# Kernel optimization log

Hardware: AMD Instinct MI355X
Metric: run time of the kernel (lower is better)

Reference implementation:

```python
import jax, jax.numpy as jnp
import numpy as np

IMG = 224
PATCH_SIZE = 2      # stride of the output patch grid (output_size = H // PATCH_SIZE)
PATCH_PIXEL = 4     # samples per patch side (deformable resampling resolution)
EMBED = 192
OFFSET_EMBED = 2    # (dx, dy) per patch
IN_CH = 3
BATCH = 32


def setup_inputs() -> dict:
    key = jax.random.key(0)
    k1, k2, k3 = jax.random.split(key, 3)
    x = jax.random.normal(k1, (BATCH, IN_CH, IMG, IMG), jnp.float32)
    conv_w = jax.random.normal(k2, (EMBED, IN_CH, 3, 3), jnp.float32) * 0.05
    conv_b = jnp.zeros((EMBED,), jnp.float32)
    off_w = jax.random.normal(k3, (OFFSET_EMBED, EMBED), jnp.float32) * 0.02
    return {"x": x, "conv_w": conv_w, "conv_b": conv_b, "off_w": off_w}


def _bilinear_gather(img, ys, xs):
    # img: [B, C, H, W]; ys, xs: [B, P] float pixel coords. Border-clamped bilinear.
    B, C, H, W = img.shape
    y0 = jnp.floor(ys)
    x0 = jnp.floor(xs)
    wy = (ys - y0)[:, None, :]
    wx = (xs - x0)[:, None, :]
    y0i = jnp.clip(y0.astype(jnp.int32), 0, H - 1)
    y1i = jnp.clip(y0i + 1, 0, H - 1)
    x0i = jnp.clip(x0.astype(jnp.int32), 0, W - 1)
    x1i = jnp.clip(x0i + 1, 0, W - 1)
    flat = img.reshape(B, C, H * W)
    P = ys.shape[1]

    def g(yi, xi):
        idx = (yi * W + xi)[:, None, :]  # [B,1,P]
        return jnp.take_along_axis(flat, jnp.broadcast_to(idx, (B, C, P)), axis=2)

    v00 = g(y0i, x0i)
    v01 = g(y0i, x1i)
    v10 = g(y1i, x0i)
    v11 = g(y1i, x1i)
    return (v00 * (1 - wy) * (1 - wx) + v01 * (1 - wy) * wx
            + v10 * wy * (1 - wx) + v11 * wy * wx)  # [B,C,P]


def reference(x, conv_w, conv_b, off_w):
    B, C, H, W = x.shape
    # PatchEmbed: conv k3 s2 p1 -> flatten -> tokens [B, N, E]
    feat = jax.lax.conv_general_dilated(
        x, conv_w, window_strides=(2, 2), padding=((1, 1), (1, 1)),
        dimension_numbers=('NCHW', 'OIHW', 'NCHW')) + conv_b[None, :, None, None]
    Hf, Wf = feat.shape[2], feat.shape[3]
    tokens = feat.reshape(B, EMBED, Hf * Wf).transpose(0, 2, 1)  # [B,N,E]
    # offset predictor: GELU (exact) then bias-free linear
    pred = jax.nn.gelu(tokens, approximate=False) @ off_w.T      # [B,N,2]

    Ho, Wo = H // PATCH_SIZE, W // PATCH_SIZE  # == (Hf, Wf) by construction
    off = pred.reshape(B, Ho, Wo, OFFSET_EMBED) * PATCH_SIZE     # pixel-space offsets

    # Deformable patch resampling: each output patch samples a PATCH_PIXEL^2 grid
    # centered at its shifted patch center.
    cy = (jnp.arange(Ho, dtype=jnp.float32) + 0.5) * PATCH_SIZE
    cx = (jnp.arange(Wo, dtype=jnp.float32) + 0.5) * PATCH_SIZE
    local = ((jnp.arange(PATCH_PIXEL, dtype=jnp.float32) + 0.5) / PATCH_PIXEL
             * PATCH_SIZE - PATCH_SIZE / 2)
    ys = (cy[None, :, None, None, None] + off[..., 1][:, :, :, None, None]
          + local[None, None, None, :, None])
    xs = (cx[None, None, :, None, None] + off[..., 0][:, :, :, None, None]
          + local[None, None, None, None, :])
    shape5 = (B, Ho, Wo, PATCH_PIXEL, PATCH_PIXEL)
    ys = jnp.broadcast_to(ys, shape5).reshape(B, -1)
    xs = jnp.broadcast_to(xs, shape5).reshape(B, -1)

    sampled = _bilinear_gather(x, ys, xs)  # [B,C,Ho*Wo*pp*pp]
    out = sampled.reshape(B, C, Ho, Wo, PATCH_PIXEL, PATCH_PIXEL)
    out = out.transpose(0, 1, 2, 4, 3, 5).reshape(
        B, C, Ho * PATCH_PIXEL, Wo * PATCH_PIXEL)
    return out
```

## Files before the change

### kernel.cpp

```cpp
#include <hip/hip_runtime.h>

#define IMG   224
#define IMG2  (IMG * IMG)
#define HO    112
#define WO_   112
#define EMBED 192
#define BATCH 32
#define PPB   (HO * WO_)
#define NPOS  (BATCH * PPB)

#define OFFS_BYTES ((size_t)NPOS * 8)
#define BT_DWORDS  (768 * 4)
#define PK_BYTES   (BT_DWORDS * 4 + 16 * 24 * 4)

typedef __attribute__((ext_vector_type(8))) short short8;
typedef __attribute__((ext_vector_type(4))) float float4v;
typedef __attribute__((ext_vector_type(2))) float float2v;
typedef __attribute__((ext_vector_type(4))) unsigned uint4v;

__device__ __forceinline__ short f2bf(float f) {
    unsigned u = __builtin_bit_cast(unsigned, f);
    u += 0x7FFFu + ((u >> 16) & 1u);
    return (short)(u >> 16);
}
__device__ __forceinline__ unsigned pack2bf(float lo, float hi) {
    return (unsigned)(unsigned short)f2bf(lo)
         | ((unsigned)(unsigned short)f2bf(hi) << 16);
}

__device__ __forceinline__ unsigned cvt_pk_bf16(float lo, float hi) {
    unsigned r;
    asm("v_cvt_pk_bf16_f32 %0, %1, %2" : "=v"(r) : "v"(lo), "v"(hi));
    return r;
}

__device__ __forceinline__ float fast_gelu(float a) {
    float e = __builtin_amdgcn_exp2f(a * -2.45546507f);
    return a * __builtin_amdgcn_rcpf(1.0f + e);
}

__device__ __forceinline__ void resample_patch(
    const float* __restrict__ xb, float* __restrict__ ob,
    int ho, int wo, int px, float ofx, float ofy)
{
    float xs  = 2.0f * wo + 0.25f + 0.5f * px + ofx;
    float x0f = floorf(xs);
    float wx  = xs - x0f;
    int x0 = (int)x0f; x0 = min(max(x0, 0), IMG - 1);
    int xq = min(x0, IMG - 2);
    bool selx = (x0 > xq);
    int ocol = wo * 4 + px;

#pragma unroll
    for (int py = 0; py < 4; ++py) {
        float ys  = 2.0f * ho + 0.25f + 0.5f * py + ofy;
        float y0f = floorf(ys);
        float wy  = ys - y0f;
        int y0 = (int)y0f; y0 = min(max(y0, 0), IMG - 1);
        int dyo = (y0 < IMG - 1) ? IMG : 0;
        int rb = y0 * IMG + xq;
        int orow = (ho * 4 + py) * 448 + ocol;

#pragma unroll
        for (int c = 0; c < 3; ++c) {
            int v0 = rb + c * IMG2;
            int v1 = v0 + dyo;
            float A0 = xb[v0], A1 = xb[v0 + 1];
            float B0 = xb[v1], B1 = xb[v1 + 1];
            float v00 = selx ? A1 : A0;
            float v10 = selx ? B1 : B0;
            float top = fmaf(wx, A1 - v00, v00);
            float bot = fmaf(wx, B1 - v10, v10);
            ob[c * 200704 + orow] = fmaf(wy, bot - top, top);
        }
    }
}

__global__ void pack_kernel(const float* __restrict__ conv_w,
                            const float* __restrict__ conv_b,
                            const float* __restrict__ off_w,
                            unsigned* __restrict__ pk) {
    int tid = threadIdx.x;
    for (int t = tid; t < 768; t += 256) {
        int nt = t >> 6, quad = (t >> 4) & 3, col = t & 15;
        int ch = nt * 16 + col;
        uint4v d;
#pragma unroll
        for (int jj = 0; jj < 4; ++jj) {
            int k0 = quad * 8 + 2 * jj, k1 = k0 + 1;
            float v0 = (k0 < 27) ? conv_w[ch * 27 + k0]
                                 : ((k0 == 27) ? conv_b[ch] : 0.0f);
            float v1 = (k1 < 27) ? conv_w[ch * 27 + k1]
                                 : ((k1 == 27) ? conv_b[ch] : 0.0f);
            d[jj] = pack2bf(v0, v1);
        }
        ((uint4v*)pk)[t] = d;
    }
    float* ow = (float*)(pk + BT_DWORDS);
    for (int t = tid; t < 384; t += 256) {
        int col = t / 24, e = t % 24;
        float v = (e < 12) ? off_w[e * 16 + col]
                           : off_w[EMBED + (e - 12) * 16 + col];
        ow[t] = v * 2.0f;
    }
}

__global__ __launch_bounds__(256)
void offsets_kernel(const float* __restrict__ x,
                    const unsigned* __restrict__ pk,
                    float2v* __restrict__ offs) {
    const int lane = threadIdx.x & 63;
    const int wv   = threadIdx.x >> 6;
    const int col  = lane & 15;
    const int quad = lane >> 4;

    const int b = blockIdx.x / (PPB / 64);
    const int p = (blockIdx.x % (PPB / 64)) * 64 + wv * 16;
    const float* __restrict__ xb = x + (size_t)b * 3 * IMG2;

    int  offj[8];
    bool isr[8], k27[8];
#pragma unroll
    for (int j = 0; j < 8; ++j) {
        int k = quad * 8 + j;
        int c = k / 9, r9 = k % 9;
        int dy = r9 / 3, dx = r9 % 3;
        isr[j] = (k < 27);
        k27[j] = (k == 27);
        offj[j] = isr[j] ? (c * IMG2 + dy * IMG + dx) : 0;
    }

    const uint4v* bT = (const uint4v*)pk;
    short8 bfrag[12];
#pragma unroll
    for (int nt = 0; nt < 12; ++nt)
        bfrag[nt] = __builtin_bit_cast(short8, bT[(nt * 4 + quad) * 16 + col]);
    const float4v* oT = (const float4v*)(pk + BT_DWORDS) + col * 6;
    float4v w0 = oT[0], w1 = oT[1], w2 = oT[2];
    float4v w3 = oT[3], w4 = oT[4], w5 = oT[5];
    float owx[12], owy[12];
#pragma unroll
    for (int i = 0; i < 4; ++i) {
        owx[i] = w0[i]; owx[4 + i] = w1[i]; owx[8 + i] = w2[i];
        owy[i] = w3[i]; owy[4 + i] = w4[i]; owy[8 + i] = w5[i];
    }

    const int ho  = p / WO_;
    const int wo0 = p % WO_;
    int iy0 = 2 * ho - 1;
    int ixl = 2 * (wo0 + col) - 1;
    int base = iy0 * IMG + ixl;

    float v[8];
    if (ho > 0 && wo0 > 0) {
#pragma unroll
        for (int j = 0; j < 8; ++j) {
            float t = isr[j] ? xb[base + offj[j]] : 0.0f;
            v[j] = k27[j] ? 1.0f : t;
        }
    } else {
#pragma unroll
        for (int j = 0; j < 8; ++j) {
            int k  = quad * 8 + j;
            int r9 = k % 9;
            int dy = r9 / 3, dx = r9 % 3;
            bool ok = isr[j] && (iy0 + dy >= 0) && (ixl + dx >= 0);
            int ad = ok ? (base + offj[j]) : 0;
            float t = ok ? xb[ad] : 0.0f;
            v[j] = k27[j] ? 1.0f : t;
        }
    }
    uint4v au = {cvt_pk_bf16(v[0], v[1]), cvt_pk_bf16(v[2], v[3]),
                 cvt_pk_bf16(v[4], v[5]), cvt_pk_bf16(v[6], v[7])};
    short8 a = __builtin_bit_cast(short8, au);

    float ox[4] = {0, 0, 0, 0}, oy[4] = {0, 0, 0, 0};
#pragma unroll
    for (int nt = 0; nt < 12; ++nt) {
        float4v c = {0.0f, 0.0f, 0.0f, 0.0f};
        c = __builtin_amdgcn_mfma_f32_16x16x32_bf16(a, bfrag[nt], c, 0, 0, 0);
#pragma unroll
        for (int r = 0; r < 4; ++r) {
            float g = fast_gelu(c[r]);
            ox[r] = fmaf(g, owx[nt], ox[r]);
            oy[r] = fmaf(g, owy[nt], oy[r]);
        }
    }
#pragma unroll
    for (int d = 1; d < 16; d <<= 1) {
#pragma unroll
        for (int r = 0; r < 4; ++r) {
            ox[r] += __shfl_xor(ox[r], d, 64);
            oy[r] += __shfl_xor(oy[r], d, 64);
        }
    }

    int rsel = col & 3;
    float sx01 = (rsel & 1) ? ox[1] : ox[0];
    float sx23 = (rsel & 1) ? ox[3] : ox[2];
    float vx   = (rsel & 2) ? sx23 : sx01;
    float sy01 = (rsel & 1) ? oy[1] : oy[0];
    float sy23 = (rsel & 1) ? oy[3] : oy[2];
    float vy   = (rsel & 2) ? sy23 : sy01;
    if (col < 4) {
        int gpos = blockIdx.x * 64 + wv * 16 + quad * 4 + rsel;
        float2v o; o[0] = vx; o[1] = vy;
        offs[gpos] = o;
    }
}

__global__ __launch_bounds__(256, 8)
void resample_kernel(const float* __restrict__ x,
                     const float2v* __restrict__ offs,
                     float* __restrict__ out) {
    const int lane  = threadIdx.x & 63;
    const int wv    = threadIdx.x >> 6;
    const int patch = lane >> 2;
    const int px    = lane & 3;

    const int b  = blockIdx.x / (PPB / 64);
    const int sb = (blockIdx.x % (PPB / 64)) * 64 + wv * 16;
    const int ho  = sb / WO_;
    const int wo0 = sb % WO_;

    const float* __restrict__ xb = x + (size_t)b * 3 * IMG2;
    float* __restrict__ ob = out + (size_t)b * 3 * (448 * 448);

    float2v o = offs[blockIdx.x * 64 + wv * 16 + patch];
    resample_patch(xb, ob, ho, wo0 + patch, px, o[0], o[1]);
}

__global__ __launch_bounds__(128)
void fused_kernel(const float* __restrict__ x,
                  const float* __restrict__ conv_w,
                  const float* __restrict__ conv_b,
                  const float* __restrict__ off_w,
                  float* __restrict__ out) {
    const int lane = threadIdx.x & 63;
    const int wv   = threadIdx.x >> 6;
    const int col  = lane & 15;
    const int quad = lane >> 4;

    const int b   = blockIdx.x / (PPB / 128);
    const int pb0 = (blockIdx.x % (PPB / 128)) * 128 + wv * 64;
    const float* __restrict__ xb = x + (size_t)b * 3 * IMG2;
    float* __restrict__ ob = out + (size_t)b * 3 * (448 * 448);

    int  offj[8];
    bool isr[8], k27[8];
#pragma unroll
    for (int j = 0; j < 8; ++j) {
        int k = quad * 8 + j;
        int c = k / 9, r9 = k % 9;
        int dy = r9 / 3, dx = r9 % 3;
        isr[j] = (k < 27);
        k27[j] = (k == 27);
        offj[j] = isr[j] ? (c * IMG2 + dy * IMG + dx) : 0;
    }
    short8 bfrag[12];
#pragma unroll
    for (int nt = 0; nt < 12; ++nt) {
        int ch = nt * 16 + col;
#pragma unroll
        for (int j = 0; j < 8; ++j) {
            int k = quad * 8 + j;
            float v = (k < 27) ? conv_w[ch * 27 + k]
                               : ((k == 27) ? conv_b[ch] : 0.0f);
            bfrag[nt][j] = f2bf(v);
        }
    }
    float owx[12], owy[12];
#pragma unroll
    for (int nt = 0; nt < 12; ++nt) {
        owx[nt] = off_w[nt * 16 + col] * 2.0f;
        owy[nt] = off_w[EMBED + nt * 16 + col] * 2.0f;
    }

    for (int it = 0; it < 4; ++it) {
        int p   = pb0 + it * 16;
        int ho  = p / WO_;
        int wo0 = p % WO_;
        int iy0 = 2 * ho - 1;
        int ixl = 2 * (wo0 + col) - 1;
        int base = iy0 * IMG + ixl;

        short8 a;
        if (ho > 0 && wo0 > 0) {
#pragma unroll
            for (int j = 0; j < 8; ++j) {
                float v = isr[j] ? xb[base + offj[j]] : 0.0f;
                if (k27[j]) v = 1.0f;
                a[j] = f2bf(v);
            }
        } else {
#pragma unroll
            for (int j = 0; j < 8; ++j) {
                int k  = quad * 8 + j;
                int r9 = k % 9;
                int dy = r9 / 3, dx = r9 % 3;
                bool ok = isr[j] && (iy0 + dy >= 0) && (ixl + dx >= 0);
                int ad = ok ? (base + offj[j]) : 0;
                float v = ok ? xb[ad] : 0.0f;
                if (k27[j]) v = 1.0f;
                a[j] = f2bf(v);
            }
        }

        float ox[4] = {0, 0, 0, 0}, oy[4] = {0, 0, 0, 0};
#pragma unroll
        for (int nt = 0; nt < 12; ++nt) {
            float4v c = {0.0f, 0.0f, 0.0f, 0.0f};
            c = __builtin_amdgcn_mfma_f32_16x16x32_bf16(a, bfrag[nt], c, 0, 0, 0);
#pragma unroll
            for (int r = 0; r < 4; ++r) {
                float g = fast_gelu(c[r]);
                ox[r] = fmaf(g, owx[nt], ox[r]);
                oy[r] = fmaf(g, owy[nt], oy[r]);
            }
        }
#pragma unroll
        for (int d = 1; d < 16; d <<= 1) {
#pragma unroll
            for (int r = 0; r < 4; ++r) {
                ox[r] += __shfl_xor(ox[r], d, 64);
                oy[r] += __shfl_xor(oy[r], d, 64);
            }
        }

        int patch = lane >> 2;
        int rsel  = patch & 3;
        int px    = lane & 3;
        float sx01 = (rsel & 1) ? ox[1] : ox[0];
        float sx23 = (rsel & 1) ? ox[3] : ox[2];
        float ofx  = (rsel & 2) ? sx23 : sx01;
        float sy01 = (rsel & 1) ? oy[1] : oy[0];
        float sy23 = (rsel & 1) ? oy[3] : oy[2];
        float ofy  = (rsel & 2) ? sy23 : sy01;

        resample_patch(xb, ob, ho, wo0 + patch, px, ofx, ofy);
    }
}

extern "C" void kernel_launch(void* const* d_in, const int* in_sizes, int n_in,
                              void* d_out, int out_size, void* d_ws, size_t ws_size,
                              hipStream_t stream) {
    const float* x      = (const float*)d_in[0];
    const float* conv_w = (const float*)d_in[1];
    const float* conv_b = (const float*)d_in[2];
    const float* off_w  = (const float*)d_in[3];
    float* out = (float*)d_out;

    const size_t need = OFFS_BYTES + PK_BYTES;
    if (d_ws != nullptr && ws_size >= need) {
        float2v* offs = (float2v*)d_ws;
        unsigned* pk  = (unsigned*)((char*)d_ws + OFFS_BYTES);
        pack_kernel<<<1, 256, 0, stream>>>(conv_w, conv_b, off_w, pk);
        offsets_kernel<<<NPOS / 64, 256, 0, stream>>>(x, pk, offs);
        resample_kernel<<<NPOS / 64, 256, 0, stream>>>(x, offs, out);
    } else {
        fused_kernel<<<NPOS / 128, 128, 0, stream>>>(x, conv_w, conv_b, off_w, out);
    }
}
```

Measured before the change: 145.8 us.

## Fuse offset prediction and deformable resampling into one kernel

Merges the offsets kernel and the resample kernel into a single kernel. Each lane takes its patch's offset straight from the reduced MFMA/GELU results in registers and calls resample_patch itself. This removes the global round trip of the per-position offset buffer and one kernel launch, and shrinks the workspace requirement. In exchange, the fused kernel carries the register pressure of both phases, which may lower occupancy for the memory-bound resampling part.

After: 138.4 us. 1.05x faster.

```diff
diff --git a/kernel.cpp b/kernel.cpp
--- a/kernel.cpp
+++ b/kernel.cpp
@@ -9,7 +9,6 @@
 #define PPB   (HO * WO_)
 #define NPOS  (BATCH * PPB)
 
-#define OFFS_BYTES ((size_t)NPOS * 8)
 #define BT_DWORDS  (768 * 4)
 #define PK_BYTES   (BT_DWORDS * 4 + 16 * 24 * 4)
 
@@ -106,9 +105,9 @@
 }
 
 __global__ __launch_bounds__(256)
-void offsets_kernel(const float* __restrict__ x,
-                    const unsigned* __restrict__ pk,
-                    float2v* __restrict__ offs) {
+void fused1_kernel(const float* __restrict__ x,
+                   const unsigned* __restrict__ pk,
+                   float* __restrict__ out) {
     const int lane = threadIdx.x & 63;
     const int wv   = threadIdx.x >> 6;
     const int col  = lane & 15;
@@ -117,6 +116,7 @@
     const int b = blockIdx.x / (PPB / 64);
     const int p = (blockIdx.x % (PPB / 64)) * 64 + wv * 16;
     const float* __restrict__ xb = x + (size_t)b * 3 * IMG2;
+    float* __restrict__ ob = out + (size_t)b * 3 * (448 * 448);
 
     int  offj[8];
     bool isr[8], k27[8];
@@ -195,39 +195,17 @@
         }
     }
 
-    int rsel = col & 3;
+    int patch = lane >> 2;
+    int rsel  = patch & 3;
+    int px    = lane & 3;
     float sx01 = (rsel & 1) ? ox[1] : ox[0];
     float sx23 = (rsel & 1) ? ox[3] : ox[2];
-    float vx   = (rsel & 2) ? sx23 : sx01;
+    float ofx  = (rsel & 2) ? sx23 : sx01;
     float sy01 = (rsel & 1) ? oy[1] : oy[0];
     float sy23 = (rsel & 1) ? oy[3] : oy[2];
-    float vy   = (rsel & 2) ? sy23 : sy01;
-    if (col < 4) {
-        int gpos = blockIdx.x * 64 + wv * 16 + quad * 4 + rsel;
-        float2v o; o[0] = vx; o[1] = vy;
-        offs[gpos] = o;
-    }
-}
-
-__global__ __launch_bounds__(256, 8)
-void resample_kernel(const float* __restrict__ x,
-                     const float2v* __restrict__ offs,
-                     float* __restrict__ out) {
-    const int lane  = threadIdx.x & 63;
-    const int wv    = threadIdx.x >> 6;
-    const int patch = lane >> 2;
-    const int px    = lane & 3;
-
-    const int b  = blockIdx.x / (PPB / 64);
-    const int sb = (blockIdx.x % (PPB / 64)) * 64 + wv * 16;
-    const int ho  = sb / WO_;
-    const int wo0 = sb % WO_;
-
-    const float* __restrict__ xb = x + (size_t)b * 3 * IMG2;
-    float* __restrict__ ob = out + (size_t)b * 3 * (448 * 448);
-
-    float2v o = offs[blockIdx.x * 64 + wv * 16 + patch];
-    resample_patch(xb, ob, ho, wo0 + patch, px, o[0], o[1]);
+    float ofy  = (rsel & 2) ? sy23 : sy01;
+
+    resample_patch(xb, ob, ho, wo0 + patch, px, ofx, ofy);
 }
 
 __global__ __launch_bounds__(128)
@@ -350,13 +328,10 @@
     const float* off_w  = (const float*)d_in[3];
     float* out = (float*)d_out;
 
-    const size_t need = OFFS_BYTES + PK_BYTES;
-    if (d_ws != nullptr && ws_size >= need) {
-        float2v* offs = (float2v*)d_ws;
-        unsigned* pk  = (unsigned*)((char*)d_ws + OFFS_BYTES);
+    if (d_ws != nullptr && ws_size >= (size_t)PK_BYTES) {
+        unsigned* pk = (unsigned*)d_ws;
         pack_kernel<<<1, 256, 0, stream>>>(conv_w, conv_b, off_w, pk);
-        offsets_kernel<<<NPOS / 64, 256, 0, stream>>>(x, pk, offs);
-        resample_kernel<<<NPOS / 64, 256, 0, stream>>>(x, offs, out);
+        fused1_kernel<<<NPOS / 64, 256, 0, stream>>>(x, pk, out);
     } else {
         fused_kernel<<<NPOS / 128, 128, 0, stream>>>(x, conv_w, conv_b, off_w, out);
     }
```
